# Kernel tuning notes

Hardware: AMD Instinct MI355X
Metric: run time of the kernel (lower is better)

## Reference

```python
import jax, jax.numpy as jnp
import numpy as np

# Dimensions
F = 512      # features = len(in_degrees)
D = 64
S, B, N = 1, 64, 256   # outer sample dim, hyper-batch, points per batch element
C = 128      # conditioner (phi) feature dim
P = F * F + F  # flat params per batch element: weight + bias


def _mask():
    # hidden-layer MADE degrees: arange(F) % max(1, D-1) + min(1, D-1)
    d = jnp.arange(F) % (D - 1) + 1
    # MaskedLinear hidden mask: out_degrees[:, None] >= in_degrees[None, :]
    # (the torch code reshapes the square [F,F] mask, which is an identity
    #  memory reshape, so element (i, j) = (d[i] >= d[j]))
    return (d[:, None] >= d[None, :]).astype(jnp.float32)


def setup_inputs() -> dict:
    key = jax.random.key(0)
    k1, k2, k3, k4 = jax.random.split(key, 4)
    return {
        "inputs": jax.random.normal(k1, (S, B, N, F), jnp.float32),
        "phi": jax.random.normal(k2, (S, B, C), jnp.float32),
        "Wc": jax.random.normal(k3, (P, C), jnp.float32) * 0.02,
        "bc": jax.random.normal(k4, (P,), jnp.float32) * 0.02,
    }


def reference(inputs, phi, Wc, bc):
    # Conditioner net: linear hypernetwork phi -> flat per-batch params.
    params = jnp.einsum('sbc,pc->sbp', phi, Wc) + bc          # [S,B,P]
    w = params[..., : F * F].reshape(S, B, F, F)               # [S,B,F_in,F_out]
    b = params[..., F * F : F * F + F]                         # [S,B,F]
    mw = w * _mask()                                           # masked per-batch weights

    # Residual block (no batch norm, dropout p=0): act -> masked linear (x2) -> residual
    t = jax.nn.relu(inputs)
    t = jnp.einsum('sbni,sbik->sbnk', t, mw) + b[:, :, None, :]
    t = jax.nn.relu(t)
    # Both MaskedLinear layers split the SAME conditioner output, so they share
    # (w, b); only the masks could differ, and with these degrees they coincide.
    t = jnp.einsum('sbni,sbik->sbnk', t, mw) + b[:, :, None, :]
    return inputs + t
```

## Files before the change

### kernel.cpp

```cpp
#include <hip/hip_runtime.h>

#define F_   512
#define FF_  (512 * 512)
#define C_   128

typedef __attribute__((ext_vector_type(4))) float f32x4;
typedef __attribute__((ext_vector_type(8))) short s16x8;
typedef __attribute__((ext_vector_type(4))) unsigned short u16x4;

__device__ __forceinline__ unsigned short f2bf(float f) {
    union { float f; unsigned u; } v; v.f = f;
    unsigned r = v.u + 0x7fffu + ((v.u >> 16) & 1u);
    return (unsigned short)(r >> 16);
}

__device__ __forceinline__ s16x8 pack8(f32x4 lo, f32x4 hi) {
    s16x8 r;
    r[0] = (short)f2bf(lo[0]); r[1] = (short)f2bf(lo[1]);
    r[2] = (short)f2bf(lo[2]); r[3] = (short)f2bf(lo[3]);
    r[4] = (short)f2bf(hi[0]); r[5] = (short)f2bf(hi[1]);
    r[6] = (short)f2bf(hi[2]); r[7] = (short)f2bf(hi[3]);
    return r;
}

#define GLDS16(gp, lp)                                                         \
    __builtin_amdgcn_global_load_lds(                                          \
        (const __attribute__((address_space(1))) void*)(gp),                   \
        (__attribute__((address_space(3))) void*)(lp), 16, 0, 0)

__global__ __launch_bounds__(256, 4) void k1_params(
    const float* __restrict__ phi, const float* __restrict__ Wc,
    const float* __restrict__ bc, unsigned short* __restrict__ wT,
    float* __restrict__ biasWS)
{
    const int blk = blockIdx.x;
    const int tid = threadIdx.x;

    if (blk >= 2048) {
        int g = ((blk - 2048) << 8) + tid;
        int k = g >> 6, b = g & 63;
        const f32x4* w4 = (const f32x4*)(Wc + (size_t)(FF_ + k) * C_);
        const f32x4* p4 = (const f32x4*)(phi + b * C_);
        float acc = bc[FF_ + k];
#pragma unroll
        for (int c = 0; c < 32; ++c) {
            f32x4 a = w4[c], q = p4[c];
            acc += a[0]*q[0] + a[1]*q[1] + a[2]*q[2] + a[3]*q[3];
        }
        biasWS[(b << 9) + k] = acc;
        return;
    }

    __shared__ __align__(16) float stg[2][2048];
    __shared__ __align__(16) unsigned short trans[64 * 136];

    const int lane = tid & 63, wave = tid >> 6;
    const int i0 = (blk >> 6) << 4;
    const int k0 = (blk & 63) << 3;

    {
        s16x8 z = {0,0,0,0,0,0,0,0};
#pragma unroll
        for (int j = 0; j < 5; ++j) {
            int idx = (j << 8) + tid;
            if (idx < 1088) *(s16x8*)&trans[idx * 8] = z;
        }
    }

    unsigned skipm = 0;
    {
        int kmin = 63;
#pragma unroll
        for (int kk = 0; kk < 8; ++kk) { int dk = (k0 + kk) % 63; kmin = dk < kmin ? dk : kmin; }
#pragma unroll
        for (int ct = 0; ct < 8; ++ct) {
            int a  = (i0 + 2 * ct) % 63;
            int b2 = (i0 + 2 * ct + 1) % 63;
            int imax = a > b2 ? a : b2;
            if (imax < kmin) skipm |= 1u << ct;
        }
    }

    const int quad = lane >> 4;
    s16x8 afr[4];
    {
        const int brow = (wave << 4) + (lane & 15);
        const int cb   = quad << 3;
#pragma unroll
        for (int kk = 0; kk < 4; ++kk) {
            const float* p = phi + brow * C_ + kk * 32 + cb;
            afr[kk] = pack8(*(const f32x4*)p, *(const f32x4*)(p + 4));
        }
    }

    const int c16 = lane & 15;
    const int di  = c16 >> 3, kq = c16 & 7;
    const int kcur = k0 + kq;
    const int dk   = kcur % 63;

    float bcv[8];
#pragma unroll
    for (int ct = 0; ct < 8; ++ct)
        bcv[ct] = bc[(i0 + ct * 2 + di) * F_ + kcur];

    const int rl8   = (wave << 1) + (lane >> 5);
    const int s16   = lane & 31;
    const int sb32  = (s16 >> 1) ^ rl8;
    const int shalf = s16 & 1;

    auto STAGE = [&](int ct, int buf) {
#pragma unroll
        for (int d = 0; d < 2; ++d) {
            const float* src = Wc
                + ((size_t)((i0 + ct * 2 + d) * F_ + k0 + rl8)) * C_
                + sb32 * 8 + shalf * 4;
            GLDS16(src, (char*)&stg[buf][(d << 10) + (wave << 8)]);
        }
    };

    bool curst = !(skipm & 1u);
    if (curst) STAGE(0, 0);

    for (int ct = 0; ct < 8; ++ct) {
        const int  bufA   = ct & 1;
        const bool nextst = (ct < 7) && !((skipm >> (ct + 1)) & 1u);
        if (nextst) STAGE(ct + 1, bufA ^ 1);
        if (curst) {
            if (nextst) asm volatile("s_waitcnt vmcnt(2)" ::: "memory");
            else        asm volatile("s_waitcnt vmcnt(0)" ::: "memory");
        }
        __builtin_amdgcn_s_barrier();
        if (curst) {
            f32x4 acc = (f32x4){0.f, 0.f, 0.f, 0.f};
            const float* sb = stg[bufA];
#pragma unroll
            for (int kk = 0; kk < 4; ++kk) {
                int off = c16 * 128 + ((((kk << 2) + quad) ^ kq) << 3);
                s16x8 bfr = pack8(*(const f32x4*)&sb[off],
                                  *(const f32x4*)&sb[off + 4]);
                acc = __builtin_amdgcn_mfma_f32_16x16x32_bf16(
                    afr[kk], bfr, acc, 0, 0, 0);
            }
            const int  icur = i0 + ct * 2 + di;
            const bool keep = (icur % 63) >= dk;
            const int  ii   = ct * 2 + di;
            const float bv  = bcv[ct];
#pragma unroll
            for (int r = 0; r < 4; ++r) {
                int b = (wave << 4) + (quad << 2) + r;
                unsigned short hv = keep ? f2bf(acc[r] + bv) : (unsigned short)0;
                trans[b * 136 + (kq << 4) + ii] = hv;
            }
        }
        __builtin_amdgcn_s_barrier();
        curst = nextst;
    }
    __syncthreads();

#pragma unroll
    for (int j = 0; j < 4; ++j) {
        int q = (j << 8) + tid;
        int b = q >> 4, kq2 = (q >> 1) & 7, h = q & 1;
        s16x8 v = *(const s16x8*)&trans[b * 136 + (kq2 << 4) + (h << 3)];
        *(s16x8*)&wT[(((size_t)((b << 9) + k0 + kq2)) << 9) + i0 + (h << 3)] = v;
    }
}

#define SMEM_BOFF 66560
#define CHUNK_B   32768
#define SMEM_TOT  (66560 + 2 * 32768)

__global__ __launch_bounds__(512) void k2_apply(
    const float* __restrict__ X, const unsigned short* __restrict__ wT,
    const float* __restrict__ biasWS, float* __restrict__ out)
{
    extern __shared__ char smem[];
    unsigned short* A_lds = (unsigned short*)smem;

    const int blk = blockIdx.x;
    const int sw  = ((blk & 7) << 5) + (blk >> 3);
    const int b   = sw >> 2;
    const int n0  = (sw & 3) << 6;

    const int tid = threadIdx.x, lane = tid & 63, wave = tid >> 6;
    const int wn = wave >> 2, wk = wave & 3;

    const float* Xb = X + (((size_t)(b * 256 + n0)) << 9);
    float*       Ob = out + (((size_t)(b * 256 + n0)) << 9);
    const unsigned short* wTb = wT + ((size_t)b << 18);

    float biasr[8];
#pragma unroll
    for (int nt = 0; nt < 8; ++nt)
        biasr[nt] = biasWS[(b << 9) + (wk << 7) + (nt << 4) + (lane & 15)];

    {
        const f32x4* X4 = (const f32x4*)Xb;
#pragma unroll
        for (int j = 0; j < 16; ++j) {
            int f = (j << 9) + tid;
            int row = f >> 7, c4 = f & 127;
            f32x4 v = X4[f];
            u16x4 h;
#pragma unroll
            for (int e = 0; e < 4; ++e) h[e] = f2bf(fmaxf(v[e], 0.f));
            *(u16x4*)&A_lds[row * 520 + (c4 << 2)] = h;
        }
    }

    const int srcslot = ((lane & 3) ^ ((lane >> 3) & 3)) << 3;

    f32x4 acc[2][8];

    for (int phase = 0; phase < 2; ++phase) {
#pragma unroll
        for (int mt = 0; mt < 2; ++mt)
#pragma unroll
            for (int nt = 0; nt < 8; ++nt) acc[mt][nt] = (f32x4){0.f, 0.f, 0.f, 0.f};

#pragma unroll
        for (int g = 0; g < 4; ++g) {
            int krow = (wave << 6) + (g << 4) + (lane >> 2);
            const unsigned short* src = wTb + ((size_t)krow << 9) + srcslot;
            char* lp = smem + SMEM_BOFF + (((wave << 6) + (g << 4)) << 6);
            GLDS16(src, lp);
        }
        asm volatile("s_waitcnt vmcnt(0)" ::: "memory");
        __syncthreads();

        for (int c = 0; c < 16; ++c) {
            const int cur = c & 1;
            if (c < 15) {
                const int i0n = (c + 1) << 5;
#pragma unroll
                for (int g = 0; g < 4; ++g) {
                    int krow = (wave << 6) + (g << 4) + (lane >> 2);
                    const unsigned short* src = wTb + ((size_t)krow << 9) + i0n + srcslot;
                    char* lp = smem + SMEM_BOFF + (cur ^ 1) * CHUNK_B
                             + (((wave << 6) + (g << 4)) << 6);
                    GLDS16(src, lp);
                }
            }
            const int i0c = c << 5;
            s16x8 afr[2];
#pragma unroll
            for (int mt = 0; mt < 2; ++mt) {
                int n = (wn << 5) + (mt << 4) + (lane & 15);
                afr[mt] = *(const s16x8*)&A_lds[n * 520 + i0c + ((lane >> 4) << 3)];
            }
            const unsigned short* Bb =
                (const unsigned short*)(smem + SMEM_BOFF + cur * CHUNK_B);
#pragma unroll
            for (int nt = 0; nt < 8; ++nt) {
                int k = (wk << 7) + (nt << 4) + (lane & 15);
                int slot = (((lane >> 4) ^ ((k >> 1) & 3)) << 3);
                s16x8 bfr = *(const s16x8*)&Bb[(k << 5) + slot];
#pragma unroll
                for (int mt = 0; mt < 2; ++mt)
                    acc[mt][nt] = __builtin_amdgcn_mfma_f32_16x16x32_bf16(
                        afr[mt], bfr, acc[mt][nt], 0, 0, 0);
            }
            asm volatile("s_waitcnt vmcnt(0)" ::: "memory");
            __syncthreads();
        }

        if (phase == 0) {
#pragma unroll
            for (int mt = 0; mt < 2; ++mt)
#pragma unroll
                for (int nt = 0; nt < 8; ++nt) {
                    int k = (wk << 7) + (nt << 4) + (lane & 15);
#pragma unroll
                    for (int r = 0; r < 4; ++r) {
                        int n = (wn << 5) + (mt << 4) + ((lane >> 4) << 2) + r;
                        A_lds[n * 520 + k] =
                            f2bf(fmaxf(acc[mt][nt][r] + biasr[nt], 0.f));
                    }
                }
            __syncthreads();
        }
    }

#pragma unroll
    for (int mt = 0; mt < 2; ++mt)
#pragma unroll
        for (int nt = 0; nt < 8; ++nt) {
            int k = (wk << 7) + (nt << 4) + (lane & 15);
#pragma unroll
            for (int r = 0; r < 4; ++r) {
                int n = (wn << 5) + (mt << 4) + ((lane >> 4) << 2) + r;
                size_t off = ((size_t)n << 9) + k;
                Ob[off] = Xb[off] + acc[mt][nt][r] + biasr[nt];
            }
        }
}

extern "C" void kernel_launch(void* const* d_in, const int* in_sizes, int n_in,
                              void* d_out, int out_size, void* d_ws, size_t ws_size,
                              hipStream_t stream) {
    const float* inputs = (const float*)d_in[0];
    const float* phi    = (const float*)d_in[1];
    const float* Wc     = (const float*)d_in[2];
    const float* bc     = (const float*)d_in[3];
    float* out = (float*)d_out;

    unsigned short* wT = (unsigned short*)d_ws;
    float* biasWS = (float*)((char*)d_ws + (size_t)64 * 512 * 512 * 2);

    hipLaunchKernelGGL(k1_params, dim3(2176), dim3(256), 0, stream,
                       phi, Wc, bc, wT, biasWS);

    hipFuncSetAttribute((const void*)k2_apply,
                        hipFuncAttributeMaxDynamicSharedMemorySize, SMEM_TOT);
    hipLaunchKernelGGL(k2_apply, dim3(256), dim3(512), SMEM_TOT, stream,
                       inputs, wT, biasWS, out);
}
```

Before: 73.14 us.

## Load conditioner weights directly into registers instead of double-buffered LDS staging

The hypernetwork weight-generation kernel no longer stages Wc tiles through a double-buffered LDS area with async global-to-LDS loads and per-step barriers. Each lane now reads its own Wc row slice straight from global memory into registers and feeds the MFMA. Masked output columns skip the load through a per-lane keep mask, which replaces the block-level skip mask. The transpose buffer is padded to a new stride so the upfront zero-fill and the barriers inside the loop can be dropped. The trade-off is more scattered, less coalesced global loads and no explicit load-compute overlap.

After: 110.7 us. 1.51x slower.

```diff
diff --git a/kernel.cpp b/kernel.cpp
--- a/kernel.cpp
+++ b/kernel.cpp
@@ -51,46 +51,20 @@
         return;
     }
 
-    __shared__ __align__(16) float stg[2][2048];
-    __shared__ __align__(16) unsigned short trans[64 * 136];
-
-    const int lane = tid & 63, wave = tid >> 6;
+    __shared__ __align__(16) unsigned short trans[64 * 192];
+
+    const int lane = tid & 63, wave = tid >> 6, quad = lane >> 4;
     const int i0 = (blk >> 6) << 4;
     const int k0 = (blk & 63) << 3;
 
-    {
-        s16x8 z = {0,0,0,0,0,0,0,0};
-#pragma unroll
-        for (int j = 0; j < 5; ++j) {
-            int idx = (j << 8) + tid;
-            if (idx < 1088) *(s16x8*)&trans[idx * 8] = z;
-        }
-    }
-
-    unsigned skipm = 0;
-    {
-        int kmin = 63;
-#pragma unroll
-        for (int kk = 0; kk < 8; ++kk) { int dk = (k0 + kk) % 63; kmin = dk < kmin ? dk : kmin; }
-#pragma unroll
-        for (int ct = 0; ct < 8; ++ct) {
-            int a  = (i0 + 2 * ct) % 63;
-            int b2 = (i0 + 2 * ct + 1) % 63;
-            int imax = a > b2 ? a : b2;
-            if (imax < kmin) skipm |= 1u << ct;
-        }
-    }
-
-    const int quad = lane >> 4;
     s16x8 afr[4];
     {
         const int brow = (wave << 4) + (lane & 15);
-        const int cb   = quad << 3;
-#pragma unroll
-        for (int kk = 0; kk < 4; ++kk) {
-            const float* p = phi + brow * C_ + kk * 32 + cb;
-            afr[kk] = pack8(*(const f32x4*)p, *(const f32x4*)(p + 4));
-        }
+        const float* p0 = phi + brow * C_ + (quad << 3);
+#pragma unroll
+        for (int kk = 0; kk < 4; ++kk)
+            afr[kk] = pack8(*(const f32x4*)(p0 + kk * 32),
+                            *(const f32x4*)(p0 + kk * 32 + 4));
     }
 
     const int c16 = lane & 15;
@@ -98,62 +72,49 @@
     const int kcur = k0 + kq;
     const int dk   = kcur % 63;
 
+    unsigned keepm = 0;
     float bcv[8];
 #pragma unroll
-    for (int ct = 0; ct < 8; ++ct)
-        bcv[ct] = bc[(i0 + ct * 2 + di) * F_ + kcur];
-
-    const int rl8   = (wave << 1) + (lane >> 5);
-    const int s16   = lane & 31;
-    const int sb32  = (s16 >> 1) ^ rl8;
-    const int shalf = s16 & 1;
-
-    auto STAGE = [&](int ct, int buf) {
-#pragma unroll
-        for (int d = 0; d < 2; ++d) {
-            const float* src = Wc
-                + ((size_t)((i0 + ct * 2 + d) * F_ + k0 + rl8)) * C_
-                + sb32 * 8 + shalf * 4;
-            GLDS16(src, (char*)&stg[buf][(d << 10) + (wave << 8)]);
-        }
-    };
-
-    bool curst = !(skipm & 1u);
-    if (curst) STAGE(0, 0);
-
     for (int ct = 0; ct < 8; ++ct) {
-        const int  bufA   = ct & 1;
-        const bool nextst = (ct < 7) && !((skipm >> (ct + 1)) & 1u);
-        if (nextst) STAGE(ct + 1, bufA ^ 1);
-        if (curst) {
-            if (nextst) asm volatile("s_waitcnt vmcnt(2)" ::: "memory");
-            else        asm volatile("s_waitcnt vmcnt(0)" ::: "memory");
-        }
-        __builtin_amdgcn_s_barrier();
-        if (curst) {
-            f32x4 acc = (f32x4){0.f, 0.f, 0.f, 0.f};
-            const float* sb = stg[bufA];
+        int icur = i0 + ct * 2 + di;
+        if ((icur % 63) >= dk) keepm |= 1u << ct;
+        bcv[ct] = bc[icur * F_ + kcur];
+    }
+
+    const float* wbase = Wc + (size_t)((i0 + di) * F_ + kcur) * C_ + (quad << 3);
+
+#pragma unroll
+    for (int ct = 0; ct < 8; ++ct) {
+        const float* wrow = wbase + (size_t)ct * (2 * F_ * C_);
+        const bool keep = (keepm >> ct) & 1;
+        f32x4 lo[4], hi[4];
+        if (keep) {
 #pragma unroll
             for (int kk = 0; kk < 4; ++kk) {
-                int off = c16 * 128 + ((((kk << 2) + quad) ^ kq) << 3);
-                s16x8 bfr = pack8(*(const f32x4*)&sb[off],
-                                  *(const f32x4*)&sb[off + 4]);
-                acc = __builtin_amdgcn_mfma_f32_16x16x32_bf16(
-                    afr[kk], bfr, acc, 0, 0, 0);
-            }
-            const int  icur = i0 + ct * 2 + di;
-            const bool keep = (icur % 63) >= dk;
-            const int  ii   = ct * 2 + di;
-            const float bv  = bcv[ct];
-#pragma unroll
-            for (int r = 0; r < 4; ++r) {
-                int b = (wave << 4) + (quad << 2) + r;
-                unsigned short hv = keep ? f2bf(acc[r] + bv) : (unsigned short)0;
-                trans[b * 136 + (kq << 4) + ii] = hv;
-            }
-        }
-        __builtin_amdgcn_s_barrier();
-        curst = nextst;
+                lo[kk] = *(const f32x4*)(wrow + kk * 32);
+                hi[kk] = *(const f32x4*)(wrow + kk * 32 + 4);
+            }
+        } else {
+#pragma unroll
+            for (int kk = 0; kk < 4; ++kk) {
+                lo[kk] = (f32x4){0.f, 0.f, 0.f, 0.f};
+                hi[kk] = (f32x4){0.f, 0.f, 0.f, 0.f};
+            }
+        }
+        f32x4 acc = (f32x4){0.f, 0.f, 0.f, 0.f};
+#pragma unroll
+        for (int kk = 0; kk < 4; ++kk)
+            acc = __builtin_amdgcn_mfma_f32_16x16x32_bf16(
+                afr[kk], pack8(lo[kk], hi[kk]), acc, 0, 0, 0);
+
+        const float bv = bcv[ct];
+        const int   ii = ct * 2 + di;
+#pragma unroll
+        for (int r = 0; r < 4; ++r) {
+            int b = (wave << 4) + (quad << 2) + r;
+            trans[b * 192 + kq * 24 + ii] =
+                keep ? f2bf(acc[r] + bv) : (unsigned short)0;
+        }
     }
     __syncthreads();
 
@@ -161,7 +122,7 @@
     for (int j = 0; j < 4; ++j) {
         int q = (j << 8) + tid;
         int b = q >> 4, kq2 = (q >> 1) & 7, h = q & 1;
-        s16x8 v = *(const s16x8*)&trans[b * 136 + (kq2 << 4) + (h << 3)];
+        s16x8 v = *(const s16x8*)&trans[b * 192 + kq2 * 24 + (h << 3)];
         *(s16x8*)&wT[(((size_t)((b << 9) + k0 + kq2)) << 9) + i0 + (h << 3)] = v;
     }
 }
```
